# Optimization experiments

Hardware: AMD Instinct MI355X
Metric: run time of the kernel (lower is better)

Reference implementation:

```python
import jax, jax.numpy as jnp
import numpy as np

D = 128
NHEAD = 4
HD = D // NHEAD
DFF = 2 * D
K = 3
NL = 2


def _ln(x, g, b, eps=1e-5):
    m = jnp.mean(x, axis=-1, keepdims=True)
    v = jnp.var(x, axis=-1, keepdims=True)
    return (x - m) / jnp.sqrt(v + eps) * g + b


def setup_inputs() -> dict:
    key = jax.random.key(0)
    ks = jax.random.split(key, 20)
    B, C, H, W = 2, 16, 128, 128
    inp = {
        "x": jax.random.normal(ks[0], (B, C, H, W), jnp.float32),
        "emb_w": jax.random.normal(ks[1], (D, C), jnp.float32) * (1.0 / np.sqrt(C)),
        "emb_b": jnp.zeros((D,), jnp.float32),
        "pos": jax.random.normal(ks[2], (1, K * K, D), jnp.float32) * 0.02,
        "wqkv": jax.random.normal(ks[3], (NL, 3 * D, D), jnp.float32) * (1.0 / np.sqrt(D)),
        "bqkv": jnp.zeros((NL, 3 * D), jnp.float32),
        "wo": jax.random.normal(ks[4], (NL, D, D), jnp.float32) * (1.0 / np.sqrt(D)),
        "bo": jnp.zeros((NL, D), jnp.float32),
        "ln1_g": jnp.ones((NL, D), jnp.float32),
        "ln1_b": jnp.zeros((NL, D), jnp.float32),
        "ln2_g": jnp.ones((NL, D), jnp.float32),
        "ln2_b": jnp.zeros((NL, D), jnp.float32),
        "w1": jax.random.normal(ks[5], (NL, DFF, D), jnp.float32) * (1.0 / np.sqrt(D)),
        "b1": jnp.zeros((NL, DFF), jnp.float32),
        "w2": jax.random.normal(ks[6], (NL, D, DFF), jnp.float32) * (1.0 / np.sqrt(DFF)),
        "b2": jnp.zeros((NL, D), jnp.float32),
        "lnf_g": jnp.ones((D,), jnp.float32),
        "lnf_b": jnp.zeros((D,), jnp.float32),
        "head_w": jax.random.normal(ks[7], (1, D), jnp.float32) * (1.0 / np.sqrt(D)),
        "head_b": jnp.zeros((1,), jnp.float32),
    }
    return inp


def reference(x, emb_w, emb_b, pos, wqkv, bqkv, wo, bo, ln1_g, ln1_b,
              ln2_g, ln2_b, w1, b1, w2, b2, lnf_g, lnf_b, head_w, head_b):
    B, C, H, W = x.shape
    # 1x1 conv embedding -> (B,H,W,D)
    e = jnp.einsum('bchw,dc->bhwd', x, emb_w) + emb_b
    # unfold: 3x3 windows with padding 1, kernel positions in row-major order
    ep = jnp.pad(e, ((0, 0), (1, 1), (1, 1), (0, 0)))
    wins = jnp.stack([ep[:, i:i + H, j:j + W, :]
                      for i in range(K) for j in range(K)], axis=3)  # (B,H,W,9,D)
    t = wins.reshape(B * H * W, K * K, D) + pos[0]  # (N,9,D)
    scale = 1.0 / np.sqrt(HD)

    def split_heads(a):
        return a.reshape(-1, K * K, NHEAD, HD).transpose(0, 2, 1, 3)

    for l in range(NL):
        # pre-LN self-attention
        h = _ln(t, ln1_g[l], ln1_b[l])
        qkv = h @ wqkv[l].T + bqkv[l]            # (N,9,3D)
        q, k, v = jnp.split(qkv, 3, axis=-1)
        q, k, v = split_heads(q), split_heads(k), split_heads(v)
        att = jax.nn.softmax(jnp.einsum('nhqd,nhkd->nhqk', q, k) * scale, axis=-1)
        o = jnp.einsum('nhqk,nhkd->nhqd', att, v)
        o = o.transpose(0, 2, 1, 3).reshape(-1, K * K, D)
        t = t + o @ wo[l].T + bo[l]
        # pre-LN FFN with exact GELU
        h2 = _ln(t, ln2_g[l], ln2_b[l])
        t = t + jax.nn.gelu(h2 @ w1[l].T + b1[l], approximate=False) @ w2[l].T + b2[l]

    center = t[:, (K * K) // 2, :]               # (N,D)
    center = _ln(center, lnf_g, lnf_b)
    logits = center @ head_w.T + head_b          # (N,1)
    return logits.reshape(B, H, W, 1).transpose(0, 3, 1, 2)
```

## Files before the change

### kernel.cpp

```cpp
#include <hip/hip_runtime.h>
#include <hip/hip_bf16.h>

typedef unsigned short u16;
typedef unsigned int   u32;
typedef __attribute__((ext_vector_type(8))) short bf16x8;
typedef __attribute__((ext_vector_type(4))) float f32x4;

#define NTOK 32768
#define TPB  4
#define MR   36
#define MPAD 48
#define NBLK (NTOK/TPB)

__device__ __forceinline__ float bf2f(u16 u) {
    u32 x = ((u32)u) << 16; float f; __builtin_memcpy(&f, &x, 4); return f;
}
__device__ __forceinline__ u16 f2bf(float f) {
    u32 u; __builtin_memcpy(&u, &f, 4);
    u32 r = (u + 0x7fffu + ((u >> 16) & 1u)) >> 16;
    return (u16)r;
}
__device__ __forceinline__ float wredsum(float v) {
#pragma unroll
    for (int m = 32; m >= 1; m >>= 1) v += __shfl_xor(v, m, 64);
    return v;
}

__global__ __launch_bounds__(256) void k_wconv(const float* __restrict__ wqkv, const float* __restrict__ wo,
                                               const float* __restrict__ w1, const float* __restrict__ w2,
                                               u16* __restrict__ wbf) {
    int i = blockIdx.x * 256 + threadIdx.x;
    float v;
    if (i < 98304)       v = wqkv[i];
    else if (i < 131072) v = wo[i - 98304];
    else if (i < 196608) v = w1[i - 131072];
    else                 v = w2[i - 196608];
    wbf[i] = f2bf(v);
}

__global__ __launch_bounds__(256) void k_embed(const float* __restrict__ x, const float* __restrict__ ew,
                                               const float* __restrict__ eb, float* __restrict__ e) {
    int idx = blockIdx.x * 256 + threadIdx.x;
    int d = idx & 127, pix = idx >> 7;
    int b = pix >> 14, hw = pix & 16383;
    const float* xp = x + b * 262144 + hw;
    const float* wr = ew + d * 16;
    float acc = eb[d];
#pragma unroll
    for (int c = 0; c < 16; ++c) acc += xp[c * 16384] * wr[c];
    e[idx] = acc;
}

__global__ __launch_bounds__(256) void k_build(const float* __restrict__ e, const float* __restrict__ pos,
                                               float* __restrict__ t) {
    int id = blockIdx.x * 256 + threadIdx.x;
    int c4 = (id & 31) << 2;
    int np = id >> 5;
    int p = np % 9;
    int n = np / 9;
    int b = n >> 14, h = (n >> 7) & 127, w = n & 127;
    int sh = h + p / 3 - 1, sw = w + p % 3 - 1;
    float4 v = {0.f, 0.f, 0.f, 0.f};
    if (sh >= 0 && sh < 128 && sw >= 0 && sw < 128)
        v = *(const float4*)(e + (size_t)((b << 14) + (sh << 7) + sw) * 128 + c4);
    float4 pv = *(const float4*)(pos + p * 128 + c4);
    v.x += pv.x; v.y += pv.y; v.z += pv.z; v.w += pv.w;
    *(float4*)(t + (size_t)np * 128 + c4) = v;
}

__global__ __launch_bounds__(256) void k_attn(
    float* __restrict__ t,
    const u16* __restrict__ wq, const float* __restrict__ bq,
    const u16* __restrict__ wov, const float* __restrict__ bov,
    const float* __restrict__ lg, const float* __restrict__ lb) {
    __shared__ char hb[MPAD * 256];
    __shared__ char qk[MPAD * 768];
    const int tid = threadIdx.x, lane = tid & 63, wid = tid >> 6;
    const int blk = blockIdx.x;
    const int col = lane & 15, grp = lane >> 4;

    if (tid < 192) {
        int pr = MR + (tid >> 4), pc = (tid & 15) * 16;
        f32x4 z = {0.f, 0.f, 0.f, 0.f};
        *(f32x4*)(hb + pr * 256 + (pc ^ ((pr & 7) << 4))) = z;
    }
    {
        float2 gv = ((const float2*)lg)[lane];
        float2 bv = ((const float2*)lb)[lane];
        for (int r = wid; r < MR; r += 4) {
            const float2* tr = (const float2*)(t + ((size_t)blk * MR + r) * 128);
            float2 xv = tr[lane];
            float mean = wredsum(xv.x + xv.y) * (1.f / 128.f);
            float var  = wredsum(xv.x * xv.x + xv.y * xv.y) * (1.f / 128.f) - mean * mean;
            float rstd = rsqrtf(var + 1e-5f);
            float h0 = (xv.x - mean) * rstd * gv.x + bv.x;
            float h1 = (xv.y - mean) * rstd * gv.y + bv.y;
            u32 pk = (u32)f2bf(h0) | ((u32)f2bf(h1) << 16);
            *(u32*)(hb + r * 256 + ((lane * 4) ^ ((r & 7) << 4))) = pk;
        }
    }
    __syncthreads();
    for (int nt = 0; nt < 6; ++nt) {
        int n0 = (wid * 6 + nt) * 16;
        int nr = n0 + col;
        bf16x8 bfr[4];
        const u16* wr = wq + nr * 128 + grp * 8;
#pragma unroll
        for (int ks = 0; ks < 4; ++ks) bfr[ks] = *(const bf16x8*)(wr + ks * 32);
        float bias = bq[nr];
        float scl = (n0 < 128) ? 0.17677669529663687f : 1.0f;
        for (int mt = 0; mt < 3; ++mt) {
            f32x4 acc = {0.f, 0.f, 0.f, 0.f};
#pragma unroll
            for (int ks = 0; ks < 4; ++ks) {
                int row = mt * 16 + col;
                bf16x8 a = *(const bf16x8*)(hb + row * 256 + ((ks * 64 + grp * 16) ^ ((row & 7) << 4)));
                acc = __builtin_amdgcn_mfma_f32_16x16x32_bf16(a, bfr[ks], acc, 0, 0, 0);
            }
#pragma unroll
            for (int j = 0; j < 4; ++j) {
                int R = mt * 16 + grp * 4 + j;
                float v = (acc[j] + bias) * scl;
                *(u16*)(qk + R * 768 + ((nr * 2) ^ ((R & 7) << 4))) = f2bf(v);
            }
        }
    }
    __syncthreads();
    {
        int tok = wid;
        int rb = tok * 9;
        for (int head = 0; head < 4; ++head) {
            int rq = rb + (col < 9 ? col : 0);
            bf16x8 aq = *(const bf16x8*)(qk + rq * 768 + ((head * 64 + grp * 16) ^ ((rq & 7) << 4)));
            bf16x8 bk = *(const bf16x8*)(qk + rq * 768 + ((256 + head * 64 + grp * 16) ^ ((rq & 7) << 4)));
            f32x4 z = {0.f, 0.f, 0.f, 0.f};
            f32x4 s = __builtin_amdgcn_mfma_f32_16x16x32_bf16(aq, bk, z, 0, 0, 0);
            bool jv = (col < 9);
            float att[4], red[4];
#pragma unroll
            for (int q4 = 0; q4 < 4; ++q4) red[q4] = jv ? s[q4] : -1e30f;
#pragma unroll
            for (int m = 8; m >= 1; m >>= 1)
#pragma unroll
                for (int q4 = 0; q4 < 4; ++q4) red[q4] = fmaxf(red[q4], __shfl_xor(red[q4], m, 64));
#pragma unroll
            for (int q4 = 0; q4 < 4; ++q4) att[q4] = jv ? __expf(s[q4] - red[q4]) : 0.f;
#pragma unroll
            for (int q4 = 0; q4 < 4; ++q4) red[q4] = att[q4];
#pragma unroll
            for (int m = 8; m >= 1; m >>= 1)
#pragma unroll
                for (int q4 = 0; q4 < 4; ++q4) red[q4] += __shfl_xor(red[q4], m, 64);
#pragma unroll
            for (int q4 = 0; q4 < 4; ++q4) att[q4] /= red[q4];
            int d = lane & 31, ih = lane >> 5;
            float vj[9];
#pragma unroll
            for (int j = 0; j < 9; ++j) {
                int row = rb + j;
                vj[j] = bf2f(*(const u16*)(qk + row * 768 + ((512 + head * 64 + d * 2) ^ ((row & 7) << 4))));
            }
            int srcb = ih * 16;
#pragma unroll
            for (int ip = 0; ip < 4; ++ip) {
                float oacc = 0.f;
#pragma unroll
                for (int j = 0; j < 9; ++j) oacc += __shfl(att[ip], srcb + j, 64) * vj[j];
                int row = rb + ip + ih * 4;
                *(u16*)(hb + row * 256 + ((head * 64 + d * 2) ^ ((row & 7) << 4))) = f2bf(oacc);
            }
            {
                float oacc = 0.f;
#pragma unroll
                for (int j = 0; j < 9; ++j) oacc += __shfl(att[0], 32 + j, 64) * vj[j];
                if (ih == 0) {
                    int row = rb + 8;
                    *(u16*)(hb + row * 256 + ((head * 64 + d * 2) ^ ((row & 7) << 4))) = f2bf(oacc);
                }
            }
        }
    }
    __syncthreads();
    for (int nt = 0; nt < 2; ++nt) {
        int n0 = (wid * 2 + nt) * 16;
        int nr = n0 + col;
        bf16x8 bfr[4];
        const u16* wr = wov + nr * 128 + grp * 8;
#pragma unroll
        for (int ks = 0; ks < 4; ++ks) bfr[ks] = *(const bf16x8*)(wr + ks * 32);
        float bias = bov[nr];
        for (int mt = 0; mt < 3; ++mt) {
            f32x4 acc = {0.f, 0.f, 0.f, 0.f};
#pragma unroll
            for (int ks = 0; ks < 4; ++ks) {
                int row = mt * 16 + col;
                bf16x8 a = *(const bf16x8*)(hb + row * 256 + ((ks * 64 + grp * 16) ^ ((row & 7) << 4)));
                acc = __builtin_amdgcn_mfma_f32_16x16x32_bf16(a, bfr[ks], acc, 0, 0, 0);
            }
#pragma unroll
            for (int j = 0; j < 4; ++j) {
                int R = mt * 16 + grp * 4 + j;
                if (R < MR) {
                    float* p = t + ((size_t)blk * MR + R) * 128 + nr;
                    *p = acc[j] + bias + *p;
                }
            }
        }
    }
}

__global__ __launch_bounds__(256) void k_ffn(
    float* __restrict__ t,
    const u16* __restrict__ w1w, const float* __restrict__ b1v,
    const u16* __restrict__ w2w, const float* __restrict__ b2v,
    const float* __restrict__ lg, const float* __restrict__ lb) {
    __shared__ char hb[MPAD * 256];
    __shared__ char mid[MPAD * 512];
    const int tid = threadIdx.x, lane = tid & 63, wid = tid >> 6;
    const int blk = blockIdx.x;
    const int col = lane & 15, grp = lane >> 4;

    if (tid < 192) {
        int pr = MR + (tid >> 4), pc = (tid & 15) * 16;
        f32x4 z = {0.f, 0.f, 0.f, 0.f};
        *(f32x4*)(hb + pr * 256 + (pc ^ ((pr & 7) << 4))) = z;
    }
    {
        float2 gv = ((const float2*)lg)[lane];
        float2 bv = ((const float2*)lb)[lane];
        for (int r = wid; r < MR; r += 4) {
            const float2* tr = (const float2*)(t + ((size_t)blk * MR + r) * 128);
            float2 xv = tr[lane];
            float mean = wredsum(xv.x + xv.y) * (1.f / 128.f);
            float var  = wredsum(xv.x * xv.x + xv.y * xv.y) * (1.f / 128.f) - mean * mean;
            float rstd = rsqrtf(var + 1e-5f);
            float h0 = (xv.x - mean) * rstd * gv.x + bv.x;
            float h1 = (xv.y - mean) * rstd * gv.y + bv.y;
            u32 pk = (u32)f2bf(h0) | ((u32)f2bf(h1) << 16);
            *(u32*)(hb + r * 256 + ((lane * 4) ^ ((r & 7) << 4))) = pk;
        }
    }
    __syncthreads();
    for (int nt = 0; nt < 4; ++nt) {
        int n0 = (wid * 4 + nt) * 16;
        int nr = n0 + col;
        bf16x8 bfr[4];
        const u16* wr = w1w + nr * 128 + grp * 8;
#pragma unroll
        for (int ks = 0; ks < 4; ++ks) bfr[ks] = *(const bf16x8*)(wr + ks * 32);
        float bias = b1v[nr];
        for (int mt = 0; mt < 3; ++mt) {
            f32x4 acc = {0.f, 0.f, 0.f, 0.f};
#pragma unroll
            for (int ks = 0; ks < 4; ++ks) {
                int row = mt * 16 + col;
                bf16x8 a = *(const bf16x8*)(hb + row * 256 + ((ks * 64 + grp * 16) ^ ((row & 7) << 4)));
                acc = __builtin_amdgcn_mfma_f32_16x16x32_bf16(a, bfr[ks], acc, 0, 0, 0);
            }
#pragma unroll
            for (int j = 0; j < 4; ++j) {
                int R = mt * 16 + grp * 4 + j;
                float xg = acc[j] + bias;
                float ge = xg * 0.5f * (1.f + erff(xg * 0.70710678118654752f));
                *(u16*)(mid + R * 512 + ((nr * 2) ^ ((R & 7) << 4))) = f2bf(ge);
            }
        }
    }
    __syncthreads();
    for (int nt = 0; nt < 2; ++nt) {
        int n0 = (wid * 2 + nt) * 16;
        int nr = n0 + col;
        bf16x8 bfr[8];
        const u16* wr = w2w + nr * 256 + grp * 8;
#pragma unroll
        for (int ks = 0; ks < 8; ++ks) bfr[ks] = *(const bf16x8*)(wr + ks * 32);
        float bias = b2v[nr];
        for (int mt = 0; mt < 3; ++mt) {
            f32x4 acc = {0.f, 0.f, 0.f, 0.f};
#pragma unroll
            for (int ks = 0; ks < 8; ++ks) {
                int row = mt * 16 + col;
                bf16x8 a = *(const bf16x8*)(mid + row * 512 + ((ks * 64 + grp * 16) ^ ((row & 7) << 4)));
                acc = __builtin_amdgcn_mfma_f32_16x16x32_bf16(a, bfr[ks], acc, 0, 0, 0);
            }
#pragma unroll
            for (int j = 0; j < 4; ++j) {
                int R = mt * 16 + grp * 4 + j;
                if (R < MR) {
                    float* p = t + ((size_t)blk * MR + R) * 128 + nr;
                    *p = acc[j] + bias + *p;
                }
            }
        }
    }
}

__global__ __launch_bounds__(256) void k_head(const float* __restrict__ t, const float* __restrict__ g,
                                              const float* __restrict__ b, const float* __restrict__ hw,
                                              const float* __restrict__ hbias, float* __restrict__ out) {
    int lane = threadIdx.x & 63, wid = threadIdx.x >> 6;
    int base = blockIdx.x * 16 + wid * 4;
    float2 gv = ((const float2*)g)[lane];
    float2 bv = ((const float2*)b)[lane];
    float2 wv = ((const float2*)hw)[lane];
    float hb0 = hbias[0];
    for (int it = 0; it < 4; ++it) {
        int n = base + it;
        const float2* row = (const float2*)(t + ((size_t)n * 9 + 4) * 128);
        float2 xv = row[lane];
        float mean = wredsum(xv.x + xv.y) * (1.f / 128.f);
        float var  = wredsum(xv.x * xv.x + xv.y * xv.y) * (1.f / 128.f) - mean * mean;
        float rstd = rsqrtf(var + 1e-5f);
        float v = ((xv.x - mean) * rstd * gv.x + bv.x) * wv.x +
                  ((xv.y - mean) * rstd * gv.y + bv.y) * wv.y;
        v = wredsum(v);
        if (lane == 0) out[n] = v + hb0;
    }
}

extern "C" void kernel_launch(void* const* d_in, const int* in_sizes, int n_in,
                              void* d_out, int out_size, void* d_ws, size_t ws_size,
                              hipStream_t stream) {
    (void)in_sizes; (void)n_in; (void)out_size; (void)ws_size;
    const float* x     = (const float*)d_in[0];
    const float* emb_w = (const float*)d_in[1];
    const float* emb_b = (const float*)d_in[2];
    const float* pos   = (const float*)d_in[3];
    const float* wqkv  = (const float*)d_in[4];
    const float* bqkv  = (const float*)d_in[5];
    const float* wo    = (const float*)d_in[6];
    const float* bo    = (const float*)d_in[7];
    const float* ln1g  = (const float*)d_in[8];
    const float* ln1b  = (const float*)d_in[9];
    const float* ln2g  = (const float*)d_in[10];
    const float* ln2b  = (const float*)d_in[11];
    const float* w1    = (const float*)d_in[12];
    const float* b1    = (const float*)d_in[13];
    const float* w2    = (const float*)d_in[14];
    const float* b2    = (const float*)d_in[15];
    const float* lnfg  = (const float*)d_in[16];
    const float* lnfb  = (const float*)d_in[17];
    const float* headw = (const float*)d_in[18];
    const float* headb = (const float*)d_in[19];
    float* out = (float*)d_out;

    char* ws = (char*)d_ws;
    float* e = (float*)ws;
    float* t = (float*)(ws + 16777216);
    u16* wbf = (u16*)(ws + 167772160);

    k_wconv<<<1024, 256, 0, stream>>>(wqkv, wo, w1, w2, wbf);
    k_embed<<<16384, 256, 0, stream>>>(x, emb_w, emb_b, e);
    k_build<<<36864, 256, 0, stream>>>(e, pos, t);
    for (int l = 0; l < 2; ++l) {
        k_attn<<<NBLK, 256, 0, stream>>>(t, wbf + l * 49152, bqkv + l * 384,
                                         wbf + 98304 + l * 16384, bo + l * 128,
                                         ln1g + l * 128, ln1b + l * 128);
        k_ffn<<<NBLK, 256, 0, stream>>>(t, wbf + 131072 + l * 32768, b1 + l * 256,
                                        wbf + 196608 + l * 32768, b2 + l * 128,
                                        ln2g + l * 128, ln2b + l * 128);
    }
    k_head<<<2048, 256, 0, stream>>>(t, lnfg, lnfb, headw, headb, out);
}
```

Measured before the change: 1.102 ms.

## Use MFMA for attention PV, transposed V layout, 512-thread blocks, fast GELU

The attention and FFN kernels move to 512 threads with 8 waves, which halves the per-wave output tiles in each GEMM stage. Attention now stores V transposed in its own shared buffer and computes P·V with an MFMA using bpermuted bf16 probabilities, replacing the scalar shuffle-and-FMA loop. Each wave now handles two token-head pairs, and softmax reductions use fewer shuffles. Exact erf GELU is replaced by an Abramowitz-Stegun polynomial with rcp/exp, which adds approximation error of about 1e-7.

After: 896.8 us. 18.7% less time.

```diff
diff --git a/kernel.cpp b/kernel.cpp
--- a/kernel.cpp
+++ b/kernel.cpp
@@ -12,6 +12,11 @@
 #define MPAD 48
 #define NBLK (NTOK/TPB)
 
+#define QK_OFF 0
+#define VT_OFF 24576
+#define HB_OFF 40960
+#define SM_ATTN 53248
+
 __device__ __forceinline__ float bf2f(u16 u) {
     u32 x = ((u32)u) << 16; float f; __builtin_memcpy(&f, &x, 4); return f;
 }
@@ -20,10 +25,22 @@
     u32 r = (u + 0x7fffu + ((u >> 16) & 1u)) >> 16;
     return (u16)r;
 }
+__device__ __forceinline__ u32 packbf(float a, float b) {
+    return (u32)f2bf(a) | ((u32)f2bf(b) << 16);
+}
 __device__ __forceinline__ float wredsum(float v) {
 #pragma unroll
     for (int m = 32; m >= 1; m >>= 1) v += __shfl_xor(v, m, 64);
     return v;
+}
+__device__ __forceinline__ float gelu_f(float x) {
+    float ax = fabsf(x) * 0.70710678118654752f;
+    float tt = __builtin_amdgcn_rcpf(1.0f + 0.3275911f * ax);
+    float poly = tt * (0.254829592f + tt * (-0.284496736f + tt * (1.421413741f +
+                 tt * (-1.453152027f + tt * 1.061405429f))));
+    float er = 1.0f - poly * __expf(-ax * ax);
+    er = copysignf(er, x);
+    return 0.5f * x * (1.0f + er);
 }
 
 __global__ __launch_bounds__(256) void k_wconv(const float* __restrict__ wqkv, const float* __restrict__ wo,
@@ -68,26 +85,30 @@
     *(float4*)(t + (size_t)np * 128 + c4) = v;
 }
 
-__global__ __launch_bounds__(256) void k_attn(
+__global__ __launch_bounds__(512, 6) void k_attn(
     float* __restrict__ t,
     const u16* __restrict__ wq, const float* __restrict__ bq,
     const u16* __restrict__ wov, const float* __restrict__ bov,
     const float* __restrict__ lg, const float* __restrict__ lb) {
-    __shared__ char hb[MPAD * 256];
-    __shared__ char qk[MPAD * 768];
+    __shared__ char smem[SM_ATTN];
+    char* qk = smem + QK_OFF;
+    char* vt = smem + VT_OFF;
+    char* hb = smem + HB_OFF;
     const int tid = threadIdx.x, lane = tid & 63, wid = tid >> 6;
     const int blk = blockIdx.x;
     const int col = lane & 15, grp = lane >> 4;
-
+    const f32x4 zero4 = {0.f, 0.f, 0.f, 0.f};
+
+    *(f32x4*)(vt + tid * 32) = zero4;
+    *(f32x4*)(vt + tid * 32 + 16) = zero4;
     if (tid < 192) {
         int pr = MR + (tid >> 4), pc = (tid & 15) * 16;
-        f32x4 z = {0.f, 0.f, 0.f, 0.f};
-        *(f32x4*)(hb + pr * 256 + (pc ^ ((pr & 7) << 4))) = z;
+        *(f32x4*)(hb + pr * 256 + (pc ^ ((pr & 7) << 4))) = zero4;
     }
     {
         float2 gv = ((const float2*)lg)[lane];
         float2 bv = ((const float2*)lb)[lane];
-        for (int r = wid; r < MR; r += 4) {
+        for (int r = wid; r < MR; r += 8) {
             const float2* tr = (const float2*)(t + ((size_t)blk * MR + r) * 128);
             float2 xv = tr[lane];
             float mean = wredsum(xv.x + xv.y) * (1.f / 128.f);
@@ -95,13 +116,13 @@
             float rstd = rsqrtf(var + 1e-5f);
             float h0 = (xv.x - mean) * rstd * gv.x + bv.x;
             float h1 = (xv.y - mean) * rstd * gv.y + bv.y;
-            u32 pk = (u32)f2bf(h0) | ((u32)f2bf(h1) << 16);
+            u32 pk = packbf(h0, h1);
             *(u32*)(hb + r * 256 + ((lane * 4) ^ ((r & 7) << 4))) = pk;
         }
     }
     __syncthreads();
-    for (int nt = 0; nt < 6; ++nt) {
-        int n0 = (wid * 6 + nt) * 16;
+    for (int nt = 0; nt < 3; ++nt) {
+        int n0 = (wid * 3 + nt) * 16;
         int nr = n0 + col;
         bf16x8 bfr[4];
         const u16* wr = wq + nr * 128 + grp * 8;
@@ -109,8 +130,9 @@
         for (int ks = 0; ks < 4; ++ks) bfr[ks] = *(const bf16x8*)(wr + ks * 32);
         float bias = bq[nr];
         float scl = (n0 < 128) ? 0.17677669529663687f : 1.0f;
+        bool isv = (n0 >= 256);
         for (int mt = 0; mt < 3; ++mt) {
-            f32x4 acc = {0.f, 0.f, 0.f, 0.f};
+            f32x4 acc = zero4;
 #pragma unroll
             for (int ks = 0; ks < 4; ++ks) {
                 int row = mt * 16 + col;
@@ -121,81 +143,74 @@
             for (int j = 0; j < 4; ++j) {
                 int R = mt * 16 + grp * 4 + j;
                 float v = (acc[j] + bias) * scl;
-                *(u16*)(qk + R * 768 + ((nr * 2) ^ ((R & 7) << 4))) = f2bf(v);
+                if (!isv) {
+                    *(u16*)(qk + R * 512 + ((nr * 2) ^ ((R & 7) << 4))) = f2bf(v);
+                } else if (R < MR) {
+                    int tok = R / 9, jp = R % 9;
+                    int d = nr - 256;
+                    *(u16*)(vt + tok * 4096 + (jp >> 3) * 2048 + d * 16 + (jp & 7) * 2) = f2bf(v);
+                }
+            }
+        }
+    }
+    __syncthreads();
+    for (int i = 0; i < 2; ++i) {
+        int pair = wid * 2 + i;
+        int tok = pair >> 2, head = pair & 3;
+        int rb = tok * 9;
+        int rm = rb + (col < 9 ? col : 8);
+        bf16x8 kf = *(const bf16x8*)(qk + rm * 512 + ((256 + head * 64 + grp * 16) ^ ((rm & 7) << 4)));
+        bf16x8 qf = *(const bf16x8*)(qk + rm * 512 + ((head * 64 + grp * 16) ^ ((rm & 7) << 4)));
+        f32x4 s = __builtin_amdgcn_mfma_f32_16x16x32_bf16(kf, qf, zero4, 0, 0, 0);
+        int jb = grp * 4;
+        float mx = -1e30f;
+#pragma unroll
+        for (int r = 0; r < 4; ++r) if (jb + r < 9) mx = fmaxf(mx, s[r]);
+        mx = fmaxf(mx, __shfl_xor(mx, 16, 64));
+        mx = fmaxf(mx, __shfl_xor(mx, 32, 64));
+        float e0[4], ss = 0.f;
+#pragma unroll
+        for (int r = 0; r < 4; ++r) { e0[r] = (jb + r < 9) ? __expf(s[r] - mx) : 0.f; ss += e0[r]; }
+        ss += __shfl_xor(ss, 16, 64);
+        ss += __shfl_xor(ss, 32, 64);
+        float rinv = __builtin_amdgcn_rcpf(ss);
+        u32 p0 = packbf(e0[0] * rinv, e0[1] * rinv);
+        u32 p1 = packbf(e0[2] * rinv, e0[3] * rinv);
+        int idx0 = (col + 32 * grp) * 4;
+        u32 w0 = (u32)__builtin_amdgcn_ds_bpermute(idx0, (int)p0);
+        u32 w1 = (u32)__builtin_amdgcn_ds_bpermute(idx0, (int)p1);
+        u32 w2 = (u32)__builtin_amdgcn_ds_bpermute(idx0 + 64, (int)p0);
+        u32 w3 = (u32)__builtin_amdgcn_ds_bpermute(idx0 + 64, (int)p1);
+        if (grp >= 2) { w0 = 0; w1 = 0; w2 = 0; w3 = 0; }
+        union { u32 w[4]; bf16x8 v; } bu;
+        bu.w[0] = w0; bu.w[1] = w1; bu.w[2] = w2; bu.w[3] = w3;
+#pragma unroll
+        for (int dh = 0; dh < 2; ++dh) {
+            bf16x8 af = *(const bf16x8*)(vt + tok * 4096 + (grp & 1) * 2048 + (head * 32 + dh * 16 + col) * 16);
+            f32x4 o = __builtin_amdgcn_mfma_f32_16x16x32_bf16(af, bu.v, zero4, 0, 0, 0);
+            if (col < 9) {
+                int row = rb + col;
+#pragma unroll
+                for (int r = 0; r < 4; ++r)
+                    *(u16*)(hb + row * 256 + ((head * 64 + dh * 32 + grp * 8 + r * 2) ^ ((row & 7) << 4))) = f2bf(o[r]);
             }
         }
     }
     __syncthreads();
     {
-        int tok = wid;
-        int rb = tok * 9;
-        for (int head = 0; head < 4; ++head) {
-            int rq = rb + (col < 9 ? col : 0);
-            bf16x8 aq = *(const bf16x8*)(qk + rq * 768 + ((head * 64 + grp * 16) ^ ((rq & 7) << 4)));
-            bf16x8 bk = *(const bf16x8*)(qk + rq * 768 + ((256 + head * 64 + grp * 16) ^ ((rq & 7) << 4)));
-            f32x4 z = {0.f, 0.f, 0.f, 0.f};
-            f32x4 s = __builtin_amdgcn_mfma_f32_16x16x32_bf16(aq, bk, z, 0, 0, 0);
-            bool jv = (col < 9);
-            float att[4], red[4];
-#pragma unroll
-            for (int q4 = 0; q4 < 4; ++q4) red[q4] = jv ? s[q4] : -1e30f;
-#pragma unroll
-            for (int m = 8; m >= 1; m >>= 1)
-#pragma unroll
-                for (int q4 = 0; q4 < 4; ++q4) red[q4] = fmaxf(red[q4], __shfl_xor(red[q4], m, 64));
-#pragma unroll
-            for (int q4 = 0; q4 < 4; ++q4) att[q4] = jv ? __expf(s[q4] - red[q4]) : 0.f;
-#pragma unroll
-            for (int q4 = 0; q4 < 4; ++q4) red[q4] = att[q4];
-#pragma unroll
-            for (int m = 8; m >= 1; m >>= 1)
-#pragma unroll
-                for (int q4 = 0; q4 < 4; ++q4) red[q4] += __shfl_xor(red[q4], m, 64);
-#pragma unroll
-            for (int q4 = 0; q4 < 4; ++q4) att[q4] /= red[q4];
-            int d = lane & 31, ih = lane >> 5;
-            float vj[9];
-#pragma unroll
-            for (int j = 0; j < 9; ++j) {
-                int row = rb + j;
-                vj[j] = bf2f(*(const u16*)(qk + row * 768 + ((512 + head * 64 + d * 2) ^ ((row & 7) << 4))));
-            }
-            int srcb = ih * 16;
-#pragma unroll
-            for (int ip = 0; ip < 4; ++ip) {
-                float oacc = 0.f;
-#pragma unroll
-                for (int j = 0; j < 9; ++j) oacc += __shfl(att[ip], srcb + j, 64) * vj[j];
-                int row = rb + ip + ih * 4;
-                *(u16*)(hb + row * 256 + ((head * 64 + d * 2) ^ ((row & 7) << 4))) = f2bf(oacc);
-            }
-            {
-                float oacc = 0.f;
-#pragma unroll
-                for (int j = 0; j < 9; ++j) oacc += __shfl(att[0], 32 + j, 64) * vj[j];
-                if (ih == 0) {
-                    int row = rb + 8;
-                    *(u16*)(hb + row * 256 + ((head * 64 + d * 2) ^ ((row & 7) << 4))) = f2bf(oacc);
-                }
-            }
-        }
-    }
-    __syncthreads();
-    for (int nt = 0; nt < 2; ++nt) {
-        int n0 = (wid * 2 + nt) * 16;
-        int nr = n0 + col;
-        bf16x8 bfr[4];
+        int nr = wid * 16 + col;
+        bf16x8 bw[4];
         const u16* wr = wov + nr * 128 + grp * 8;
 #pragma unroll
-        for (int ks = 0; ks < 4; ++ks) bfr[ks] = *(const bf16x8*)(wr + ks * 32);
+        for (int ks = 0; ks < 4; ++ks) bw[ks] = *(const bf16x8*)(wr + ks * 32);
         float bias = bov[nr];
         for (int mt = 0; mt < 3; ++mt) {
-            f32x4 acc = {0.f, 0.f, 0.f, 0.f};
+            f32x4 acc = zero4;
 #pragma unroll
             for (int ks = 0; ks < 4; ++ks) {
                 int row = mt * 16 + col;
                 bf16x8 a = *(const bf16x8*)(hb + row * 256 + ((ks * 64 + grp * 16) ^ ((row & 7) << 4)));
-                acc = __builtin_amdgcn_mfma_f32_16x16x32_bf16(a, bfr[ks], acc, 0, 0, 0);
+                acc = __builtin_amdgcn_mfma_f32_16x16x32_bf16(a, bw[ks], acc, 0, 0, 0);
             }
 #pragma unroll
             for (int j = 0; j < 4; ++j) {
@@ -209,26 +224,27 @@
     }
 }
 
-__global__ __launch_bounds__(256) void k_ffn(
+__global__ __launch_bounds__(512, 6) void k_ffn(
     float* __restrict__ t,
     const u16* __restrict__ w1w, const float* __restrict__ b1v,
     const u16* __restrict__ w2w, const float* __restrict__ b2v,
     const float* __restrict__ lg, const float* __restrict__ lb) {
-    __shared__ char hb[MPAD * 256];
-    __shared__ char mid[MPAD * 512];
+    __shared__ char smem[36864];
+    char* hb  = smem;
+    char* mid = smem + 12288;
     const int tid = threadIdx.x, lane = tid & 63, wid = tid >> 6;
     const int blk = blockIdx.x;
     const int col = lane & 15, grp = lane >> 4;
+    const f32x4 zero4 = {0.f, 0.f, 0.f, 0.f};
 
     if (tid < 192) {
         int pr = MR + (tid >> 4), pc = (tid & 15) * 16;
-        f32x4 z = {0.f, 0.f, 0.f, 0.f};
-        *(f32x4*)(hb + pr * 256 + (pc ^ ((pr & 7) << 4))) = z;
+        *(f32x4*)(hb + pr * 256 + (pc ^ ((pr & 7) << 4))) = zero4;
     }
     {
         float2 gv = ((const float2*)lg)[lane];
         float2 bv = ((const float2*)lb)[lane];
-        for (int r = wid; r < MR; r += 4) {
+        for (int r = wid; r < MR; r += 8) {
             const float2* tr = (const float2*)(t + ((size_t)blk * MR + r) * 128);
             float2 xv = tr[lane];
             float mean = wredsum(xv.x + xv.y) * (1.f / 128.f);
@@ -236,13 +252,13 @@
             float rstd = rsqrtf(var + 1e-5f);
             float h0 = (xv.x - mean) * rstd * gv.x + bv.x;
             float h1 = (xv.y - mean) * rstd * gv.y + bv.y;
-            u32 pk = (u32)f2bf(h0) | ((u32)f2bf(h1) << 16);
+            u32 pk = packbf(h0, h1);
             *(u32*)(hb + r * 256 + ((lane * 4) ^ ((r & 7) << 4))) = pk;
         }
     }
     __syncthreads();
-    for (int nt = 0; nt < 4; ++nt) {
-        int n0 = (wid * 4 + nt) * 16;
+    for (int nt = 0; nt < 2; ++nt) {
+        int n0 = (wid * 2 + nt) * 16;
         int nr = n0 + col;
         bf16x8 bfr[4];
         const u16* wr = w1w + nr * 128 + grp * 8;
@@ -250,7 +266,7 @@
         for (int ks = 0; ks < 4; ++ks) bfr[ks] = *(const bf16x8*)(wr + ks * 32);
         float bias = b1v[nr];
         for (int mt = 0; mt < 3; ++mt) {
-            f32x4 acc = {0.f, 0.f, 0.f, 0.f};
+            f32x4 acc = zero4;
 #pragma unroll
             for (int ks = 0; ks < 4; ++ks) {
                 int row = mt * 16 + col;
@@ -260,23 +276,21 @@
 #pragma unroll
             for (int j = 0; j < 4; ++j) {
                 int R = mt * 16 + grp * 4 + j;
-                float xg = acc[j] + bias;
-                float ge = xg * 0.5f * (1.f + erff(xg * 0.70710678118654752f));
+                float ge = gelu_f(acc[j] + bias);
                 *(u16*)(mid + R * 512 + ((nr * 2) ^ ((R & 7) << 4))) = f2bf(ge);
             }
         }
     }
     __syncthreads();
-    for (int nt = 0; nt < 2; ++nt) {
-        int n0 = (wid * 2 + nt) * 16;
-        int nr = n0 + col;
+    {
+        int nr = wid * 16 + col;
         bf16x8 bfr[8];
         const u16* wr = w2w + nr * 256 + grp * 8;
 #pragma unroll
         for (int ks = 0; ks < 8; ++ks) bfr[ks] = *(const bf16x8*)(wr + ks * 32);
         float bias = b2v[nr];
         for (int mt = 0; mt < 3; ++mt) {
-            f32x4 acc = {0.f, 0.f, 0.f, 0.f};
+            f32x4 acc = zero4;
 #pragma unroll
             for (int ks = 0; ks < 8; ++ks) {
                 int row = mt * 16 + col;
@@ -353,10 +367,10 @@
     k_embed<<<16384, 256, 0, stream>>>(x, emb_w, emb_b, e);
     k_build<<<36864, 256, 0, stream>>>(e, pos, t);
     for (int l = 0; l < 2; ++l) {
-        k_attn<<<NBLK, 256, 0, stream>>>(t, wbf + l * 49152, bqkv + l * 384,
+        k_attn<<<NBLK, 512, 0, stream>>>(t, wbf + l * 49152, bqkv + l * 384,
                                          wbf + 98304 + l * 16384, bo + l * 128,
                                          ln1g + l * 128, ln1b + l * 128);
-        k_ffn<<<NBLK, 256, 0, stream>>>(t, wbf + 131072 + l * 32768, b1 + l * 256,
+        k_ffn<<<NBLK, 512, 0, stream>>>(t, wbf + 131072 + l * 32768, b1 + l * 256,
                                         wbf + 196608 + l * 32768, b2 + l * 128,
                                         ln2g + l * 128, ln2b + l * 128);
     }
```
